# Optimization experiments

Hardware: AMD Instinct MI355X
Metric: run time of the kernel (lower is better)

## Reference

```python
import jax, jax.numpy as jnp
import numpy as np

H, QK, V, HID = 24, 16, 16, 128
EPS = 1e-6


def setup_inputs() -> dict:
    key = jax.random.key(0)
    ks = jax.random.split(key, 12)
    N, L = 2, 512
    s = 0.05
    inp = {
        "x": jax.random.normal(ks[0], (N, L, HID), jnp.float32),
        "R": jax.random.normal(ks[1], (N, L, 3, 3), jnp.float32),
        "t": jax.random.normal(ks[2], (N, L, 3), jnp.float32) * 10.0,
        "mask": jnp.ones((N, L), bool),
        # torch nn.Linear weights are (out_features, in_features)
        "Wq": jax.random.normal(ks[3], (H * QK, HID), jnp.float32) * s,
        "Wk": jax.random.normal(ks[4], (H * QK, HID), jnp.float32) * s,
        "Wv": jax.random.normal(ks[5], (H * V, HID), jnp.float32) * s,
        "bv": jnp.zeros((H * V,), jnp.float32),
        "Wa": jax.random.normal(ks[6], (3 * H, HID), jnp.float32) * s,
        "ba": jnp.full((3 * H,), EPS, jnp.float32),
        "Wb": jax.random.normal(ks[7], (3 * H, HID), jnp.float32) * s,
        "bb": jnp.full((3 * H,), EPS, jnp.float32),
        "Wp": jax.random.normal(ks[8], (HID, (V + 5) * H), jnp.float32) * s,
        "bp": jnp.zeros((HID,), jnp.float32),
        "alpha": -2.0 * jnp.ones((1, H, 1, 1), jnp.float32),
        "beta": -2.0 * jnp.ones((1, H, 1, 1), jnp.float32),
    }
    return inp


def reference(x, R, t, mask, Wq, Wk, Wv, bv, Wa, ba, Wb, bb, Wp, bp, alpha, beta):
    N, L, _ = x.shape
    al = jax.nn.softplus(alpha)  # (1,H,1,1)
    be = jax.nn.softplus(beta)

    a = (x @ Wa.T + ba).reshape(N, L, H, 1, 3).transpose(0, 2, 1, 3, 4)  # (N,H,L,1,3)
    b = (x @ Wb.T + bb).reshape(N, L, H, 1, 3).transpose(0, 2, 1, 3, 4)  # (N,H,L,1,3)

    # to_local: express t_j in local frame of residue i -> R_i^T (t_j - t_i)
    rel = t[:, None, :, :] - t[:, :, None, :]              # (N,L,L,3)
    local = jnp.einsum('nidx,nijd->nijx', R, rel)          # (N,L,L,3)

    r = local[:, None] - b                                  # (N,H,L,L,3)
    r_size = jnp.sqrt(jnp.sum(r * r, axis=-1))              # (N,H,L,L)
    a_size = jnp.sqrt(jnp.sum(a * a, axis=-1))              # (N,H,L,1)
    r_dot_a = jnp.sum(r * a, axis=-1)                       # (N,H,L,L)
    theta = jnp.arccos(r_dot_a / ((r_size + EPS) * (a_size + EPS)))

    ray_w = -al * r_size - be * theta                       # (N,H,L,L)

    q = (x @ Wq.T).reshape(N, L, H, QK)
    k = (x @ Wk.T).reshape(N, L, H, QK)
    std_w = jnp.einsum('nihd,njhd->nhij', q, k) * (QK ** -0.5)

    att = (2.0 ** -0.5) * (ray_w + std_w)
    diag = jnp.eye(L, dtype=bool)
    att = jnp.where(diag[None, None], jnp.asarray(-100.0, att.dtype), att)
    att = jnp.where(mask[:, None, None, :], att, -jnp.inf)
    att = jax.nn.softmax(att, axis=-1)                      # (N,H,L,L)

    v = (x @ Wv.T + bv).reshape(N, L, H, V)
    v_aggr = jnp.einsum('nhij,njhd->nihd', att, v)          # (N,L,H,V)
    r_aggr = jnp.einsum('nhij,nhijd->nihd', att, r)         # (N,L,H,3)
    r_aggr_size = jnp.sqrt(jnp.sum(r_aggr * r_aggr, axis=-1))  # (N,L,H)
    theta_aggr = jnp.einsum('nhij,nhij->nih', att, theta)   # (N,L,H)

    concat = jnp.concatenate([
        v_aggr.reshape(N, L, -1),
        r_aggr.reshape(N, L, -1),
        r_aggr_size,
        theta_aggr,
    ], axis=-1)                                             # (N,L,(V+5)*H)
    return concat @ Wp.T + bp
```

## Files before the change

kernel.cpp:

```cpp
#include <hip/hip_runtime.h>
#include <math.h>

#define NHEAD 24
#define LEN   512
#define NB    2
#define HID   128
#define EPSI  1e-6f

static constexpr size_t QKV_SZ = (size_t)NB * NHEAD * LEN * 16;
static constexpr size_t AB_SZ  = (size_t)NB * NHEAD * LEN * 3;
static constexpr size_t Q_OFF = 0;
static constexpr size_t K_OFF = QKV_SZ;
static constexpr size_t V_OFF = 2 * QKV_SZ;
static constexpr size_t A_OFF = 3 * QKV_SZ;
static constexpr size_t B_OFF = A_OFF + AB_SZ;
static constexpr size_t C_OFF = B_OFF + AB_SZ;

#define QSCALE2 0.25504597f
#define SCL     1.02020406f
#define CSHIFT  (-14.4269504f)

__device__ __forceinline__ float fast_exp2(float x) {
    return __builtin_amdgcn_exp2f(x);
}

__device__ __forceinline__ void store_proj(int rg, int pos, float val,
    const float* __restrict__ bv, const float* __restrict__ ba,
    const float* __restrict__ bb, float* __restrict__ ws)
{
    const int n = pos >> 9;
    const int j = pos & (LEN - 1);
    if (rg < 384) {
        const int h = rg >> 4, d = rg & 15;
        ws[Q_OFF + ((((size_t)(n*NHEAD + h))*LEN + j) << 4) + d] = val * QSCALE2;
    } else if (rg < 768) {
        const int r = rg - 384, h = r >> 4, d = r & 15;
        ws[K_OFF + ((((size_t)(n*NHEAD + h))*LEN + j) << 4) + d] = val;
    } else if (rg < 1152) {
        const int r = rg - 768, h = r >> 4, d = r & 15;
        ws[V_OFF + ((((size_t)(n*NHEAD + h))*LEN + j) << 4) + d] = val + bv[r];
    } else if (rg < 1224) {
        const int r = rg - 1152, h = r / 3, c = r - h*3;
        ws[A_OFF + (((size_t)(n*NHEAD + h))*LEN + j)*3 + c] = val + ba[r];
    } else {
        const int r = rg - 1224, h = r / 3, c = r - h*3;
        ws[B_OFF + (((size_t)(n*NHEAD + h))*LEN + j)*3 + c] = val + bb[r];
    }
}

__global__ __launch_bounds__(256) void proj_kernel(
    const float* __restrict__ x,
    const float* __restrict__ Wq, const float* __restrict__ Wk,
    const float* __restrict__ Wv, const float* __restrict__ bv,
    const float* __restrict__ Wa, const float* __restrict__ ba,
    const float* __restrict__ Wb, const float* __restrict__ bb,
    float* __restrict__ ws)
{
    __shared__ float Wsh[64][132];
    __shared__ float Xsh[32][132];
    const int tid    = threadIdx.x;
    const int r_base = blockIdx.x * 64;
    const int p_base = blockIdx.y * 32;

    #pragma unroll
    for (int it = 0; it < 8; ++it) {
        const int f = tid + 256*it;
        const int row = f >> 5, c4 = (f & 31) << 2;
        int rg = r_base + row;
        if (rg >= 1296) rg = 0;
        const float* src;
        if      (rg < 384)  src = Wq + (size_t)rg*HID;
        else if (rg < 768)  src = Wk + (size_t)(rg-384)*HID;
        else if (rg < 1152) src = Wv + (size_t)(rg-768)*HID;
        else if (rg < 1224) src = Wa + (size_t)(rg-1152)*HID;
        else                src = Wb + (size_t)(rg-1224)*HID;
        *(float4*)&Wsh[row][c4] = *(const float4*)(src + c4);
    }
    #pragma unroll
    for (int it = 0; it < 4; ++it) {
        const int f = tid + 256*it;
        const int row = f >> 5, c4 = (f & 31) << 2;
        *(float4*)&Xsh[row][c4] =
            *(const float4*)(x + (size_t)(p_base + row)*HID + c4);
    }
    __syncthreads();

    const int a0 = tid >> 4;
    const int p0 = tid & 15;

    float acc[4][2];
    #pragma unroll
    for (int m = 0; m < 4; ++m) { acc[m][0] = 0.f; acc[m][1] = 0.f; }

    #pragma unroll 2
    for (int k4 = 0; k4 < 32; ++k4) {
        float4 wv[4], xv[2];
        #pragma unroll
        for (int m = 0; m < 4; ++m) wv[m] = *(float4*)&Wsh[a0 + 16*m][k4*4];
        #pragma unroll
        for (int q = 0; q < 2; ++q) xv[q] = *(float4*)&Xsh[p0 + 16*q][k4*4];
        #pragma unroll
        for (int m = 0; m < 4; ++m)
            #pragma unroll
            for (int q = 0; q < 2; ++q)
                acc[m][q] = fmaf(wv[m].x, xv[q].x, fmaf(wv[m].y, xv[q].y,
                            fmaf(wv[m].z, xv[q].z, fmaf(wv[m].w, xv[q].w, acc[m][q]))));
    }

    #pragma unroll
    for (int m = 0; m < 4; ++m) {
        const int rg = r_base + a0 + 16*m;
        if (rg >= 1296) continue;
        #pragma unroll
        for (int q = 0; q < 2; ++q)
            store_proj(rg, p_base + p0 + 16*q, acc[m][q], bv, ba, bb, ws);
    }
}

__global__ __launch_bounds__(256) void attn_kernel(
    const float* __restrict__ Rm, const float* __restrict__ tg,
    const float* __restrict__ alpha, const float* __restrict__ beta,
    const float* __restrict__ ws, float* __restrict__ conc)
{
    __shared__ float  ks[2][64*20];
    __shared__ float  vs[2][64*20];
    __shared__ float4 ts4[2][64];

    const int tid   = threadIdx.x;
    const int lane  = tid & 63;
    const int li    = lane & 15;
    const int g     = lane >> 4;
    const int bx    = blockIdx.x;
    const int nh    = bx >> 5;
    const int ibase = (bx & 31) << 4;
    const int h     = nh % NHEAD;
    const int n     = nh / NHEAD;
    const int i     = ibase + ((tid >> 6) << 2) + g;
    const int iloc  = i & 63;
    const int dtile = ibase >> 6;

    const size_t nh16 = (size_t)nh * LEN * 16;
    const float* kg   = ws + K_OFF + nh16;
    const float* vg   = ws + V_OFF + nh16;
    const float* tng  = tg + (size_t)n * LEN * 3;

    auto stage = [&](int tt, int b) {
        const int row = tid >> 2, c4 = (tid & 3) << 2;
        *(float4*)&ks[b][row*20 + c4] = *(const float4*)(kg + (size_t)tt*1024 + tid*4);
        *(float4*)&vs[b][row*20 + c4] = *(const float4*)(vg + (size_t)tt*1024 + tid*4);
        if (tid < 64) {
            const int j = (tt << 6) + tid;
            ts4[b][tid] = make_float4(tng[j*3+0], tng[j*3+1], tng[j*3+2], 0.f);
        }
    };

    stage(0, 0);

    const size_t ni = (size_t)n * LEN + i;
    const float* Ri = Rm + ni * 9;
    const float R00 = Ri[0], R01 = Ri[1], R02 = Ri[2];
    const float R10 = Ri[3], R11 = Ri[4], R12 = Ri[5];
    const float R20 = Ri[6], R21 = Ri[7], R22 = Ri[8];
    const float ti0 = tng[i*3+0], ti1 = tng[i*3+1], ti2 = tng[i*3+2];

    const float* bpn = ws + B_OFF + ((size_t)nh*LEN + i)*3;
    const float c0 = -(R00*ti0 + R10*ti1 + R20*ti2) - bpn[0];
    const float c1 = -(R01*ti0 + R11*ti1 + R21*ti2) - bpn[1];
    const float c2 = -(R02*ti0 + R12*ti1 + R22*ti2) - bpn[2];

    const float* ap = ws + A_OFF + ((size_t)nh*LEN + i)*3;
    const float a0 = ap[0], a1 = ap[1], a2 = ap[2];
    const float inv_as = 1.0f / (sqrtf(a0*a0 + a1*a1 + a2*a2) + EPSI);
    const float an0 = a0*inv_as, an1 = a1*inv_as, an2 = a2*inv_as;

    const float4* qp = (const float4*)(ws + Q_OFF + nh16 + ((size_t)i << 4));
    const float4 q0 = qp[0], q1 = qp[1], q2 = qp[2], q3 = qp[3];

    const float al2n = -SCL * log1pf(__expf(alpha[h]));
    const float be2n = -SCL * log1pf(__expf(beta[h]));

    float ssum = 0.f, thacc = 0.f;
    float racc0 = 0.f, racc1 = 0.f, racc2 = 0.f;
    float vacc[16];
    #pragma unroll
    for (int d = 0; d < 16; ++d) vacc[d] = 0.f;

    __syncthreads();

    for (int tt = 0; tt < 8; ++tt) {
        const int cur = tt & 1;
        if (tt < 7) stage(tt + 1, cur ^ 1);
        const bool isdiag = (tt == dtile);

        #pragma unroll
        for (int sub = 0; sub < 4; ++sub) {
            const int jl = li + (sub << 4);
            const float4 tj = ts4[cur][jl];

            const float r0 = fmaf(R00,tj.x, fmaf(R10,tj.y, fmaf(R20,tj.z, c0)));
            const float r1 = fmaf(R01,tj.x, fmaf(R11,tj.y, fmaf(R21,tj.z, c1)));
            const float r2 = fmaf(R02,tj.x, fmaf(R12,tj.y, fmaf(R22,tj.z, c2)));
            const float rs  = sqrtf(fmaf(r0,r0, fmaf(r1,r1, r2*r2)));
            const float rda = fmaf(r0,an0, fmaf(r1,an1, r2*an2));
            float carg = rda * __builtin_amdgcn_rcpf(rs + EPSI);
            carg = fminf(1.f, fmaxf(-1.f, carg));
            const float u = fabsf(carg);
            const float thp = sqrtf(1.f - u) *
                (1.5707288f + u*(-0.2121144f + u*(0.0742610f - 0.0187293f*u)));
            const float theta = (carg >= 0.f) ? thp : (3.14159265f - thp);

            const float* kb = &ks[cur][jl*20];
            const float4 k0 = *(const float4*)(kb+0),  k1 = *(const float4*)(kb+4);
            const float4 k2 = *(const float4*)(kb+8),  k3 = *(const float4*)(kb+12);
            float qk = q0.x*k0.x;
            qk = fmaf(q0.y,k0.y, qk); qk = fmaf(q0.z,k0.z, qk); qk = fmaf(q0.w,k0.w, qk);
            qk = fmaf(q1.x,k1.x, qk); qk = fmaf(q1.y,k1.y, qk); qk = fmaf(q1.z,k1.z, qk); qk = fmaf(q1.w,k1.w, qk);
            qk = fmaf(q2.x,k2.x, qk); qk = fmaf(q2.y,k2.y, qk); qk = fmaf(q2.z,k2.z, qk); qk = fmaf(q2.w,k2.w, qk);
            qk = fmaf(q3.x,k3.x, qk); qk = fmaf(q3.y,k3.y, qk); qk = fmaf(q3.z,k3.z, qk); qk = fmaf(q3.w,k3.w, qk);

            float sc = fmaf(be2n, theta, fmaf(al2n, rs, qk)) + CSHIFT;
            float p  = fast_exp2(sc);
            if (isdiag && jl == iloc) p = 0.f;

            const float* vb = &vs[cur][jl*20];
            const float4 v0 = *(const float4*)(vb+0),  v1 = *(const float4*)(vb+4);
            const float4 v2 = *(const float4*)(vb+8),  v3 = *(const float4*)(vb+12);

            ssum += p;
            vacc[0]  = fmaf(p,v0.x,vacc[0]);  vacc[1]  = fmaf(p,v0.y,vacc[1]);
            vacc[2]  = fmaf(p,v0.z,vacc[2]);  vacc[3]  = fmaf(p,v0.w,vacc[3]);
            vacc[4]  = fmaf(p,v1.x,vacc[4]);  vacc[5]  = fmaf(p,v1.y,vacc[5]);
            vacc[6]  = fmaf(p,v1.z,vacc[6]);  vacc[7]  = fmaf(p,v1.w,vacc[7]);
            vacc[8]  = fmaf(p,v2.x,vacc[8]);  vacc[9]  = fmaf(p,v2.y,vacc[9]);
            vacc[10] = fmaf(p,v2.z,vacc[10]); vacc[11] = fmaf(p,v2.w,vacc[11]);
            vacc[12] = fmaf(p,v3.x,vacc[12]); vacc[13] = fmaf(p,v3.y,vacc[13]);
            vacc[14] = fmaf(p,v3.z,vacc[14]); vacc[15] = fmaf(p,v3.w,vacc[15]);
            racc0 = fmaf(p,r0,racc0); racc1 = fmaf(p,r1,racc1); racc2 = fmaf(p,r2,racc2);
            thacc = fmaf(p,theta,thacc);
        }
        __syncthreads();
    }

    #pragma unroll
    for (int msk = 1; msk < 16; msk <<= 1) {
        ssum  += __shfl_xor(ssum,  msk, 16);
        #pragma unroll
        for (int d = 0; d < 16; ++d) vacc[d] += __shfl_xor(vacc[d], msk, 16);
        racc0 += __shfl_xor(racc0, msk, 16);
        racc1 += __shfl_xor(racc1, msk, 16);
        racc2 += __shfl_xor(racc2, msk, 16);
        thacc += __shfl_xor(thacc, msk, 16);
    }

    if (li == 0) {
        const float inv = 1.0f / ssum;
        float* cb = conc + ni * 504;
        #pragma unroll
        for (int d = 0; d < 16; ++d) cb[(h<<4) + d] = vacc[d] * inv;
        const float ra0 = racc0*inv, ra1 = racc1*inv, ra2 = racc2*inv;
        cb[384 + h*3 + 0] = ra0;
        cb[384 + h*3 + 1] = ra1;
        cb[384 + h*3 + 2] = ra2;
        cb[456 + h] = sqrtf(ra0*ra0 + ra1*ra1 + ra2*ra2);
        cb[480 + h] = thacc * inv;
    }
}

__global__ __launch_bounds__(256) void outproj_kernel(
    const float* __restrict__ conc, const float* __restrict__ Wp,
    const float* __restrict__ bp, float* __restrict__ out)
{
    __shared__ float Csh[64][60];
    __shared__ float Wsh[32][60];
    const int tid    = threadIdx.x;
    const int p_base = blockIdx.x * 64;
    const int o_base = blockIdx.y * 32;
    const int kc     = blockIdx.z * 56;
    const int p0 = tid >> 4, ob = tid & 15;

    for (int f = tid; f < 64*14; f += 256) {
        const int row = f / 14, c4 = (f - row*14) << 2;
        *(float4*)&Csh[row][c4] =
            *(const float4*)(conc + (size_t)(p_base + row)*504 + kc + c4);
    }
    for (int f = tid; f < 32*14; f += 256) {
        const int row = f / 14, c4 = (f - row*14) << 2;
        *(float4*)&Wsh[row][c4] =
            *(const float4*)(Wp + (size_t)(o_base + row)*504 + kc + c4);
    }
    __syncthreads();

    float acc[4][2];
    #pragma unroll
    for (int m = 0; m < 4; ++m) { acc[m][0] = 0.f; acc[m][1] = 0.f; }

    #pragma unroll 2
    for (int k4 = 0; k4 < 14; ++k4) {
        float4 xv[4], wv[2];
        #pragma unroll
        for (int m = 0; m < 4; ++m) xv[m] = *(float4*)&Csh[p0 + 16*m][k4*4];
        #pragma unroll
        for (int o = 0; o < 2; ++o) wv[o] = *(float4*)&Wsh[ob + 16*o][k4*4];
        #pragma unroll
        for (int m = 0; m < 4; ++m)
            #pragma unroll
            for (int o = 0; o < 2; ++o)
                acc[m][o] += xv[m].x*wv[o].x + xv[m].y*wv[o].y +
                             xv[m].z*wv[o].z + xv[m].w*wv[o].w;
    }

    const bool first = (blockIdx.z == 0);
    #pragma unroll
    for (int m = 0; m < 4; ++m) {
        const int p = p_base + p0 + 16*m;
        #pragma unroll
        for (int o = 0; o < 2; ++o) {
            const int oo = o_base + ob + 16*o;
            const float add = acc[m][o] + (first ? bp[oo] : 0.f);
            atomicAdd(&out[(size_t)p*HID + oo], add);
        }
    }
}

extern "C" void kernel_launch(void* const* d_in, const int* in_sizes, int n_in,
                              void* d_out, int out_size, void* d_ws, size_t ws_size,
                              hipStream_t stream) {
    const float* x     = (const float*)d_in[0];
    const float* R     = (const float*)d_in[1];
    const float* t     = (const float*)d_in[2];
    const float* Wq    = (const float*)d_in[4];
    const float* Wk    = (const float*)d_in[5];
    const float* Wv    = (const float*)d_in[6];
    const float* bv    = (const float*)d_in[7];
    const float* Wa    = (const float*)d_in[8];
    const float* ba    = (const float*)d_in[9];
    const float* Wb    = (const float*)d_in[10];
    const float* bb    = (const float*)d_in[11];
    const float* Wp    = (const float*)d_in[12];
    const float* bp    = (const float*)d_in[13];
    const float* alpha = (const float*)d_in[14];
    const float* beta  = (const float*)d_in[15];

    float* ws  = (float*)d_ws;
    float* out = (float*)d_out;

    hipMemsetAsync(out, 0, (size_t)out_size * sizeof(float), stream);

    proj_kernel<<<dim3(21, 32), 256, 0, stream>>>(
        x, Wq, Wk, Wv, bv, Wa, ba, Wb, bb, ws);

    attn_kernel<<<(NB * NHEAD * LEN) / 16, 256, 0, stream>>>(
        R, t, alpha, beta, ws, ws + C_OFF);

    outproj_kernel<<<dim3(16, 4, 9), 256, 0, stream>>>(ws + C_OFF, Wp, bp, out);
}
```

Measured before the change: 152.5 us.

## Fuse output projection into attention kernel and shrink projection tiles

The attention kernel now computes each head's partial output projection itself. It stages the 21 relevant Wp columns per head in shared memory and atomically adds the per-head contribution into the output, so the concat buffer and the separate outproj kernel are gone. This removes one launch and a global round-trip of the concatenated features, at the cost of many more atomics (24 heads per output element) and extra per-block Wp loading. The projection kernel also switches to 32-row weight tiles with twice as many blocks, for better occupancy.

Result: faster. 147.9 us (-3.0%).

```diff
diff --git a/kernel.cpp b/kernel.cpp
--- a/kernel.cpp
+++ b/kernel.cpp
@@ -14,7 +14,6 @@
 static constexpr size_t V_OFF = 2 * QKV_SZ;
 static constexpr size_t A_OFF = 3 * QKV_SZ;
 static constexpr size_t B_OFF = A_OFF + AB_SZ;
-static constexpr size_t C_OFF = B_OFF + AB_SZ;
 
 #define QSCALE2 0.25504597f
 #define SCL     1.02020406f
@@ -56,14 +55,14 @@
     const float* __restrict__ Wb, const float* __restrict__ bb,
     float* __restrict__ ws)
 {
-    __shared__ float Wsh[64][132];
+    __shared__ float Wsh[32][132];
     __shared__ float Xsh[32][132];
     const int tid    = threadIdx.x;
-    const int r_base = blockIdx.x * 64;
+    const int r_base = blockIdx.x * 32;
     const int p_base = blockIdx.y * 32;
 
     #pragma unroll
-    for (int it = 0; it < 8; ++it) {
+    for (int it = 0; it < 4; ++it) {
         const int f = tid + 256*it;
         const int row = f >> 5, c4 = (f & 31) << 2;
         int rg = r_base + row;
@@ -88,19 +87,18 @@
     const int a0 = tid >> 4;
     const int p0 = tid & 15;
 
-    float acc[4][2];
-    #pragma unroll
-    for (int m = 0; m < 4; ++m) { acc[m][0] = 0.f; acc[m][1] = 0.f; }
-
-    #pragma unroll 2
+    float acc[2][2];
+    acc[0][0] = acc[0][1] = acc[1][0] = acc[1][1] = 0.f;
+
+    #pragma unroll 4
     for (int k4 = 0; k4 < 32; ++k4) {
-        float4 wv[4], xv[2];
-        #pragma unroll
-        for (int m = 0; m < 4; ++m) wv[m] = *(float4*)&Wsh[a0 + 16*m][k4*4];
-        #pragma unroll
-        for (int q = 0; q < 2; ++q) xv[q] = *(float4*)&Xsh[p0 + 16*q][k4*4];
-        #pragma unroll
-        for (int m = 0; m < 4; ++m)
+        float4 wv[2], xv[2];
+        wv[0] = *(float4*)&Wsh[a0     ][k4*4];
+        wv[1] = *(float4*)&Wsh[a0 + 16][k4*4];
+        xv[0] = *(float4*)&Xsh[p0     ][k4*4];
+        xv[1] = *(float4*)&Xsh[p0 + 16][k4*4];
+        #pragma unroll
+        for (int m = 0; m < 2; ++m)
             #pragma unroll
             for (int q = 0; q < 2; ++q)
                 acc[m][q] = fmaf(wv[m].x, xv[q].x, fmaf(wv[m].y, xv[q].y,
@@ -108,7 +106,7 @@
     }
 
     #pragma unroll
-    for (int m = 0; m < 4; ++m) {
+    for (int m = 0; m < 2; ++m) {
         const int rg = r_base + a0 + 16*m;
         if (rg >= 1296) continue;
         #pragma unroll
@@ -117,14 +115,18 @@
     }
 }
 
-__global__ __launch_bounds__(256) void attn_kernel(
+__global__ __launch_bounds__(256) void attn_fused_kernel(
     const float* __restrict__ Rm, const float* __restrict__ tg,
     const float* __restrict__ alpha, const float* __restrict__ beta,
-    const float* __restrict__ ws, float* __restrict__ conc)
+    const float* __restrict__ ws,
+    const float* __restrict__ Wp, const float* __restrict__ bp,
+    float* __restrict__ out)
 {
     __shared__ float  ks[2][64*20];
     __shared__ float  vs[2][64*20];
     __shared__ float4 ts4[2][64];
+    __shared__ float  Wpsh[128][24];
+    __shared__ float  sval[16][24];
 
     const int tid   = threadIdx.x;
     const int lane  = tid & 63;
@@ -135,7 +137,8 @@
     const int ibase = (bx & 31) << 4;
     const int h     = nh % NHEAD;
     const int n     = nh / NHEAD;
-    const int i     = ibase + ((tid >> 6) << 2) + g;
+    const int rloc  = ((tid >> 6) << 2) + g;
+    const int i     = ibase + rloc;
     const int iloc  = i & 63;
     const int dtile = ibase >> 6;
 
@@ -155,6 +158,16 @@
     };
 
     stage(0, 0);
+
+    for (int f = tid; f < 128*21; f += 256) {
+        const int o = f / 21, c = f - o*21;
+        int col;
+        if      (c < 16) col = (h << 4) + c;
+        else if (c < 19) col = 384 + h*3 + (c - 16);
+        else if (c == 19) col = 456 + h;
+        else              col = 480 + h;
+        Wpsh[o][c] = Wp[(size_t)o*504 + col];
+    }
 
     const size_t ni = (size_t)n * LEN + i;
     const float* Ri = Rm + ni * 9;
@@ -254,71 +267,46 @@
 
     if (li == 0) {
         const float inv = 1.0f / ssum;
-        float* cb = conc + ni * 504;
-        #pragma unroll
-        for (int d = 0; d < 16; ++d) cb[(h<<4) + d] = vacc[d] * inv;
+        float* sv = &sval[rloc][0];
+        #pragma unroll
+        for (int d = 0; d < 16; ++d) sv[d] = vacc[d] * inv;
         const float ra0 = racc0*inv, ra1 = racc1*inv, ra2 = racc2*inv;
-        cb[384 + h*3 + 0] = ra0;
-        cb[384 + h*3 + 1] = ra1;
-        cb[384 + h*3 + 2] = ra2;
-        cb[456 + h] = sqrtf(ra0*ra0 + ra1*ra1 + ra2*ra2);
-        cb[480 + h] = thacc * inv;
-    }
-}
-
-__global__ __launch_bounds__(256) void outproj_kernel(
-    const float* __restrict__ conc, const float* __restrict__ Wp,
-    const float* __restrict__ bp, float* __restrict__ out)
-{
-    __shared__ float Csh[64][60];
-    __shared__ float Wsh[32][60];
-    const int tid    = threadIdx.x;
-    const int p_base = blockIdx.x * 64;
-    const int o_base = blockIdx.y * 32;
-    const int kc     = blockIdx.z * 56;
-    const int p0 = tid >> 4, ob = tid & 15;
-
-    for (int f = tid; f < 64*14; f += 256) {
-        const int row = f / 14, c4 = (f - row*14) << 2;
-        *(float4*)&Csh[row][c4] =
-            *(const float4*)(conc + (size_t)(p_base + row)*504 + kc + c4);
-    }
-    for (int f = tid; f < 32*14; f += 256) {
-        const int row = f / 14, c4 = (f - row*14) << 2;
-        *(float4*)&Wsh[row][c4] =
-            *(const float4*)(Wp + (size_t)(o_base + row)*504 + kc + c4);
+        sv[16] = ra0;
+        sv[17] = ra1;
+        sv[18] = ra2;
+        sv[19] = sqrtf(fmaf(ra0,ra0, fmaf(ra1,ra1, ra2*ra2)));
+        sv[20] = thacc * inv;
     }
     __syncthreads();
 
-    float acc[4][2];
-    #pragma unroll
-    for (int m = 0; m < 4; ++m) { acc[m][0] = 0.f; acc[m][1] = 0.f; }
-
-    #pragma unroll 2
-    for (int k4 = 0; k4 < 14; ++k4) {
-        float4 xv[4], wv[2];
-        #pragma unroll
-        for (int m = 0; m < 4; ++m) xv[m] = *(float4*)&Csh[p0 + 16*m][k4*4];
-        #pragma unroll
-        for (int o = 0; o < 2; ++o) wv[o] = *(float4*)&Wsh[ob + 16*o][k4*4];
-        #pragma unroll
-        for (int m = 0; m < 4; ++m)
-            #pragma unroll
-            for (int o = 0; o < 2; ++o)
-                acc[m][o] += xv[m].x*wv[o].x + xv[m].y*wv[o].y +
-                             xv[m].z*wv[o].z + xv[m].w*wv[o].w;
-    }
-
-    const bool first = (blockIdx.z == 0);
-    #pragma unroll
-    for (int m = 0; m < 4; ++m) {
-        const int p = p_base + p0 + 16*m;
-        #pragma unroll
-        for (int o = 0; o < 2; ++o) {
-            const int oo = o_base + ob + 16*o;
-            const float add = acc[m][o] + (first ? bp[oo] : 0.f);
-            atomicAdd(&out[(size_t)p*HID + oo], add);
-        }
+    const int o  = tid & 127;
+    const int rh = tid >> 7;
+    const float4 w0 = *(const float4*)&Wpsh[o][0];
+    const float4 w1 = *(const float4*)&Wpsh[o][4];
+    const float4 w2 = *(const float4*)&Wpsh[o][8];
+    const float4 w3 = *(const float4*)&Wpsh[o][12];
+    const float4 w4 = *(const float4*)&Wpsh[o][16];
+    const float  w20 = Wpsh[o][20];
+    const float  bo  = (h == 0) ? bp[o] : 0.f;
+    float* outb = out + ((size_t)n * LEN + ibase) * HID + o;
+
+    #pragma unroll
+    for (int k = 0; k < 8; ++k) {
+        const int r = rh * 8 + k;
+        const float4 s0 = *(const float4*)&sval[r][0];
+        const float4 s1 = *(const float4*)&sval[r][4];
+        const float4 s2 = *(const float4*)&sval[r][8];
+        const float4 s3 = *(const float4*)&sval[r][12];
+        const float4 s4 = *(const float4*)&sval[r][16];
+        const float  s20 = sval[r][20];
+        float s = bo;
+        s = fmaf(w0.x,s0.x, fmaf(w0.y,s0.y, fmaf(w0.z,s0.z, fmaf(w0.w,s0.w, s))));
+        s = fmaf(w1.x,s1.x, fmaf(w1.y,s1.y, fmaf(w1.z,s1.z, fmaf(w1.w,s1.w, s))));
+        s = fmaf(w2.x,s2.x, fmaf(w2.y,s2.y, fmaf(w2.z,s2.z, fmaf(w2.w,s2.w, s))));
+        s = fmaf(w3.x,s3.x, fmaf(w3.y,s3.y, fmaf(w3.z,s3.z, fmaf(w3.w,s3.w, s))));
+        s = fmaf(w4.x,s4.x, fmaf(w4.y,s4.y, fmaf(w4.z,s4.z, fmaf(w4.w,s4.w, s))));
+        s = fmaf(w20, s20, s);
+        atomicAdd(outb + (size_t)r * HID, s);
     }
 }
 
@@ -346,11 +334,9 @@
 
     hipMemsetAsync(out, 0, (size_t)out_size * sizeof(float), stream);
 
-    proj_kernel<<<dim3(21, 32), 256, 0, stream>>>(
+    proj_kernel<<<dim3(41, 32), 256, 0, stream>>>(
         x, Wq, Wk, Wv, bv, Wa, ba, Wb, bb, ws);
 
-    attn_kernel<<<(NB * NHEAD * LEN) / 16, 256, 0, stream>>>(
-        R, t, alpha, beta, ws, ws + C_OFF);
-
-    outproj_kernel<<<dim3(16, 4, 9), 256, 0, stream>>>(ws + C_OFF, Wp, bp, out);
-}
+    attn_fused_kernel<<<(NB * NHEAD * LEN) / 16, 256, 0, stream>>>(
+        R, t, alpha, beta, ws, Wp, bp, out);
+}
```
